# Kernel optimization log

Hardware: AMD Instinct MI355X
Metric: run time of the kernel (lower is better)

Reference implementation:

```python
import jax, jax.numpy as jnp
import numpy as np

N_NODES = 100000
N_EDGES = 1600000
NUM_GRAPHS = 64
IN_CH, HID, NUM_CLASSES = 128, 64, 10


def _glorot(key, fan_in, fan_out):
    scale = jnp.sqrt(2.0 / (fan_in + fan_out)).astype(jnp.float32)
    return jax.random.normal(key, (fan_in, fan_out), jnp.float32) * scale


def setup_inputs() -> dict:
    key = jax.random.key(0)
    ks = jax.random.split(key, 7)
    x = jax.random.normal(ks[0], (N_NODES, IN_CH), jnp.float32)
    edge_index = jax.random.randint(ks[1], (2, N_EDGES), 0, N_NODES, dtype=jnp.int32)
    batch = jnp.sort(jax.random.randint(ks[2], (N_NODES,), 0, NUM_GRAPHS, dtype=jnp.int32))
    return {
        "x": x,
        "edge_index": edge_index,
        "batch": batch,
        "W1": _glorot(ks[3], IN_CH, HID), "b1": jnp.zeros((HID,), jnp.float32),
        "W2": _glorot(ks[4], HID, HID), "b2": jnp.zeros((HID,), jnp.float32),
        "W3": _glorot(ks[5], HID, NUM_CLASSES), "b3": jnp.zeros((NUM_CLASSES,), jnp.float32),
    }


def _gcn_conv(x, src, dst, norm, W, b):
    # GCNConv: h = X W, then symmetric-normalized scatter-add over edges, then + b
    h = x @ W                                  # [N, out]
    msg = norm[:, None] * h[src]               # [E+N, out] gather
    out = jax.ops.segment_sum(msg, dst, num_segments=N_NODES)
    return out + b


def reference(x, edge_index, batch, W1, b1, W2, b2, W3, b3):
    loop = jnp.arange(N_NODES, dtype=edge_index.dtype)
    src = jnp.concatenate([edge_index[0], loop])   # self-loops added (PyG gcn_norm)
    dst = jnp.concatenate([edge_index[1], loop])
    deg = jax.ops.segment_sum(jnp.ones(src.shape[0], x.dtype), dst, num_segments=N_NODES)
    dinv = jnp.where(deg > 0, jax.lax.rsqrt(deg), jnp.zeros_like(deg))
    norm = dinv[src] * dinv[dst]

    h = jax.nn.relu(_gcn_conv(x, src, dst, norm, W1, b1))  # dropout is identity in eval
    h = jax.nn.relu(_gcn_conv(h, src, dst, norm, W2, b2))
    h = _gcn_conv(h, src, dst, norm, W3, b3)

    counts = jax.ops.segment_sum(jnp.ones(N_NODES, h.dtype), batch, num_segments=NUM_GRAPHS)
    pooled = jax.ops.segment_sum(h, batch, num_segments=NUM_GRAPHS) / jnp.maximum(counts, 1.0)[:, None]
    return jax.nn.log_softmax(pooled, axis=1)
```

## Files before the change

### kernel.cpp

```cpp
#include <hip/hip_runtime.h>
#include <math.h>

#define IN_CH 128
#define HID   64
#define NC    10
#define BSH   8
#define NBLK  256

typedef unsigned short bfu;
typedef __attribute__((ext_vector_type(8))) short bf16x8;
typedef __attribute__((ext_vector_type(4))) float f32x4;
typedef __attribute__((ext_vector_type(2))) float f32x2;

static __device__ __forceinline__ bfu bf16_of(float f) {
    unsigned u = __float_as_uint(f);
    unsigned r = (u + 0x7FFF + ((u >> 16) & 1)) >> 16;
    return (bfu)r;
}
static __device__ __forceinline__ float f_of_bf16(bfu u) {
    return __uint_as_float(((unsigned)u) << 16);
}

#if __has_builtin(__builtin_amdgcn_cvt_pk_f32_fp8) && __has_builtin(__builtin_amdgcn_cvt_pk_fp8_f32)
template <bool HI>
static __device__ __forceinline__ f32x2 fp8_unpk(unsigned d) {
    return __builtin_amdgcn_cvt_pk_f32_fp8((int)d, HI);
}
template <bool HI>
static __device__ __forceinline__ int fp8_pk(float a, float b, int old) {
    return __builtin_amdgcn_cvt_pk_fp8_f32(a, b, old, HI);
}
#else
static __device__ __forceinline__ float fp8_dec1(unsigned b) {
    unsigned s = b >> 7, e = (b >> 3) & 15, m = b & 7;
    float v = (e == 0) ? ldexpf((float)m, -9) : ldexpf((float)(8 + m), (int)e - 10);
    return s ? -v : v;
}
static __device__ __forceinline__ unsigned fp8_enc1(float f) {
    unsigned u = __float_as_uint(f);
    unsigned s = (u >> 31) << 7;
    f = fabsf(f);
    if (!(f < 448.f)) return s | 0x7E;
    if (f < 0.015625f) {
        int q = (int)rintf(f * 512.f);
        return s | (unsigned)q;
    }
    int e; float fr = frexpf(f, &e);
    int q = (int)rintf(fr * 16.f);
    if (q == 16) { q = 8; e++; }
    int E = e + 6;
    if (E >= 16) return s | 0x7E;
    return s | (unsigned)((E << 3) | (q - 8));
}
template <bool HI>
static __device__ __forceinline__ f32x2 fp8_unpk(unsigned d) {
    unsigned w = HI ? (d >> 16) : d;
    f32x2 r; r.x = fp8_dec1(w & 0xFF); r.y = fp8_dec1((w >> 8) & 0xFF);
    return r;
}
template <bool HI>
static __device__ __forceinline__ int fp8_pk(float a, float b, int old) {
    unsigned p = fp8_enc1(a) | (fp8_enc1(b) << 8);
    return HI ? (int)(((unsigned)old & 0x0000FFFFu) | (p << 16))
              : (int)(((unsigned)old & 0xFFFF0000u) | p);
}
#endif

__device__ __forceinline__ int lower_bound_i(const int* a, int n, int v) {
    int lo = 0, hi = n;
    while (lo < hi) { int mid = (lo + hi) >> 1; if (a[mid] < v) lo = mid + 1; else hi = mid; }
    return lo;
}


__global__ void k_init(int* __restrict__ cnt, float* __restrict__ Psum,
                       unsigned* __restrict__ dumA, unsigned* __restrict__ dumB,
                       int nbuck, int ng) {
    int t = threadIdx.x;
    for (int i = t; i < nbuck; i += 512) cnt[i] = 0;
    for (int i = t; i < ng * HID; i += 512) Psum[i] = 0.f;
    if (t < 16) { dumA[t] = 0u; dumB[t] = 0u; }
}


__global__ __launch_bounds__(1024) void k_part(const int* __restrict__ src,
                                               const int* __restrict__ dst,
                                               int* __restrict__ cnt,
                                               unsigned* __restrict__ packed,
                                               int E, int nbuck, int chunk, int cap) {
    __shared__ int hist[512];
    int tid = threadIdx.x;
    for (int b = tid; b < nbuck; b += 1024) hist[b] = 0;
    __syncthreads();
    int base = blockIdx.x * chunk;
    int lim  = min(base + chunk, E);
    for (int e = base + tid; e < lim; e += 1024)
        atomicAdd(&hist[dst[e] >> BSH], 1);
    __syncthreads();
    for (int b = tid; b < nbuck; b += 1024) {
        int c = hist[b];
        hist[b] = c ? atomicAdd(&cnt[b], c) : 0;
    }
    __syncthreads();
    for (int e = base + tid; e < lim; e += 1024) {
        int d = dst[e], s = src[e];
        int b = d >> BSH;
        int pos = atomicAdd(&hist[b], 1);
        if (pos < cap)
            packed[(size_t)b * (size_t)cap + pos] = ((unsigned)s << 8) | (unsigned)(d & 255);
    }
}


__global__ __launch_bounds__(512) void k_placeC(const unsigned* __restrict__ packed,
                                                const int* __restrict__ cnt,
                                                int2* __restrict__ rp2,
                                                float* __restrict__ dinv,
                                                int* __restrict__ meta,
                                                int nn, int cap, int capm) {
    __shared__ int hist[256];
    __shared__ int scn[256];
    __shared__ int cur[256];
    int tid = threadIdx.x;
    int b   = blockIdx.x;
    int nb0 = b << BSH;
    int nnb = min(1 << BSH, nn - nb0);
    if (tid < 256) hist[tid] = 0;
    __syncthreads();
    int lo = b * cap;
    int hi = lo + min(cnt[b], cap);
    for (int e = lo + tid; e < hi; e += blockDim.x)
        atomicAdd(&hist[packed[e] & 255u], 1);
    __syncthreads();
    int pd = 0;
    if (tid < 256) { pd = (hist[tid] + 3) & ~3; scn[tid] = pd; }
    __syncthreads();
    for (int off = 1; off < 256; off <<= 1) {
        int t = 0;
        if (tid < 256 && tid >= off) t = scn[tid - off];
        __syncthreads();
        if (tid < 256) scn[tid] += t;
        __syncthreads();
    }
    int meta0 = b * capm;
    if (tid < nnb) {
        int rp = meta0 + scn[tid] - pd;
        rp2[nb0 + tid] = make_int2(rp, rp + pd);
        cur[tid] = rp;
        dinv[nb0 + tid] = rsqrtf((float)(hist[tid] + 1));
        for (int k = hist[tid]; k < pd; k++) meta[rp + k] = nn;
    }
    __syncthreads();
    for (int e = lo + tid; e < hi; e += blockDim.x) {
        unsigned p = packed[e];
        int pos = atomicAdd(&cur[p & 255u], 1);
        meta[pos] = (int)(p >> 8);
    }
}


template <int K, bool IN_BF16>
__global__ __launch_bounds__(256) void k_gemm(const void* __restrict__ Xv,
                                              const float* __restrict__ W,
                                              const float* __restrict__ dinv,
                                              unsigned char* __restrict__ G8, int n) {
    constexpr int KS = K + 8;
    __shared__ bfu wt[64 * KS];
    int tid = threadIdx.x;
    for (int i = tid; i < K * 64; i += 256) {
        int k = i >> 6, nn2 = i & 63;
        wt[nn2 * KS + k] = bf16_of(W[i]);
    }
    __syncthreads();
    int wave = tid >> 6, lane = tid & 63;
    int m = lane & 15, q = lane >> 4;
    int row0 = blockIdx.x * 64 + wave * 16;
    int rowA = min(row0 + m, n - 1);
    f32x4 acc[4] = {{0.f,0.f,0.f,0.f},{0.f,0.f,0.f,0.f},
                    {0.f,0.f,0.f,0.f},{0.f,0.f,0.f,0.f}};
#pragma unroll
    for (int ks = 0; ks < K / 32; ks++) {
        bf16x8 a;
        if (IN_BF16) {
            a = *(const bf16x8*)((const bfu*)Xv + (size_t)rowA * 64 + ks * 32 + q * 8);
        } else {
            const float* xp = (const float*)Xv + (size_t)rowA * K + ks * 32 + q * 8;
            float4 v0 = *(const float4*)xp;
            float4 v1 = *(const float4*)(xp + 4);
            union { unsigned u[4]; bf16x8 v; } cvt;
            cvt.u[0] = __builtin_amdgcn_perm(__float_as_uint(v0.y), __float_as_uint(v0.x), 0x07060302u);
            cvt.u[1] = __builtin_amdgcn_perm(__float_as_uint(v0.w), __float_as_uint(v0.z), 0x07060302u);
            cvt.u[2] = __builtin_amdgcn_perm(__float_as_uint(v1.y), __float_as_uint(v1.x), 0x07060302u);
            cvt.u[3] = __builtin_amdgcn_perm(__float_as_uint(v1.w), __float_as_uint(v1.z), 0x07060302u);
            a = cvt.v;
        }
#pragma unroll
        for (int nt = 0; nt < 4; nt++) {
            bf16x8 b = *(const bf16x8*)&wt[(nt * 16 + m) * KS + ks * 32 + q * 8];
            acc[nt] = __builtin_amdgcn_mfma_f32_16x16x32_bf16(a, b, acc[nt], 0, 0, 0);
        }
    }
#pragma unroll
    for (int r = 0; r < 4; r++) {
        int grow = row0 + q * 4 + r;
        if (grow < n) {
            float dv = dinv[grow];
            int p01 = fp8_pk<false>(acc[0][r] * dv, acc[1][r] * dv, 0);
            int p23 = fp8_pk<false>(acc[2][r] * dv, acc[3][r] * dv, 0);
            unsigned char* gp = G8 + (size_t)grow * 64 + m;
            gp[0]  = (unsigned char)(p01 & 0xFF);
            gp[16] = (unsigned char)((p01 >> 8) & 0xFF);
            gp[32] = (unsigned char)(p23 & 0xFF);
            gp[48] = (unsigned char)((p23 >> 8) & 0xFF);
        }
    }
}


template <int MODE>
__global__ void k_agg(const unsigned* __restrict__ G4, const int* __restrict__ meta,
                      const int2* __restrict__ rp2, const float* __restrict__ dinv,
                      const float* __restrict__ bias, void* __restrict__ outv,
                      const int* __restrict__ batch, float* __restrict__ Psum,
                      int n, int ng, int do_relu, int post_scale) {
    __shared__ float pw[16][64];
    __shared__ int sb[16];
    int tid = threadIdx.x;
    int wbase = ((blockIdx.x * blockDim.x + tid) >> 6) * 4;
    if (MODE != 2) { if (wbase >= n) return; }
    int lane = tid & 63;
    int col4 = lane & 15, equad = lane >> 4;
    int nb0 = blockIdx.x * 16;
    if (MODE == 2 && tid < 16)
        sb[tid] = (nb0 + tid < n) ? batch[nb0 + tid] : -1;
    int nd    = wbase + equad;
    bool alive = nd < n;
    int ndc   = alive ? nd : (n - 1);
    int2 rp = rp2[ndc];
    int beg = rp.x, pend = alive ? rp.y : rp.x;
    f32x2 aA = {0.f, 0.f}, aB = {0.f, 0.f};
    for (int e = beg; e < pend; e += 4) {
        int4 m = *(const int4*)&meta[e];
        unsigned d0 = G4[(size_t)m.x * 16 + col4];
        unsigned d1 = G4[(size_t)m.y * 16 + col4];
        unsigned d2 = G4[(size_t)m.z * 16 + col4];
        unsigned d3 = G4[(size_t)m.w * 16 + col4];
        aA += fp8_unpk<false>(d0); aB += fp8_unpk<true>(d0);
        aA += fp8_unpk<false>(d1); aB += fp8_unpk<true>(d1);
        aA += fp8_unpk<false>(d2); aB += fp8_unpk<true>(d2);
        aA += fp8_unpk<false>(d3); aB += fp8_unpk<true>(d3);
    }
    unsigned sv = G4[(size_t)ndc * 16 + col4];
    aA += fp8_unpk<false>(sv); aB += fp8_unpk<true>(sv);
    float dv = dinv[ndc];
    float a0 = aA.x * dv, a1 = aA.y * dv, a2 = aB.x * dv, a3 = aB.y * dv;
    if (bias) {
        float4 bv = *(const float4*)&bias[col4 * 4];
        a0 += bv.x; a1 += bv.y; a2 += bv.z; a3 += bv.w;
    }
    if (do_relu) {
        a0 = fmaxf(a0, 0.f); a1 = fmaxf(a1, 0.f);
        a2 = fmaxf(a2, 0.f); a3 = fmaxf(a3, 0.f);
    }
    if (post_scale) { a0 *= dv; a1 *= dv; a2 *= dv; a3 *= dv; }
    if (MODE == 2) {
        int slot = (tid >> 6) * 4 + equad;
        f32x4 st;
        st.x = alive ? a0 : 0.f; st.y = alive ? a1 : 0.f;
        st.z = alive ? a2 : 0.f; st.w = alive ? a3 : 0.f;
        *(f32x4*)&pw[slot][col4 * 4] = st;
        __syncthreads();
        int r = tid >> 6, c = tid & 63;
        int g0 = sb[0];
        float v = 0.f;
#pragma unroll
        for (int s2 = 0; s2 < 16; s2++)
            if (sb[s2] == g0 + r) v += pw[s2][c];
        if (v != 0.f && g0 + r < ng) atomicAdd(&Psum[(g0 + r) * 64 + c], v);
        if (tid < 16) {
            int bb = sb[tid];
            if (bb > g0 + 3) {
                for (int c2 = 0; c2 < 64; c2++)
                    atomicAdd(&Psum[bb * 64 + c2], pw[tid][c2]);
            }
        }
    } else if (alive) {
        if (MODE == 1) {
            int p = fp8_pk<false>(a0, a1, 0);
            p = fp8_pk<true>(a2, a3, p);
            ((unsigned*)outv)[(size_t)nd * 16 + col4] = (unsigned)p;
        } else {
            uint2 o;
            o.x = (unsigned)bf16_of(a0) | ((unsigned)bf16_of(a1) << 16);
            o.y = (unsigned)bf16_of(a2) | ((unsigned)bf16_of(a3) << 16);
            ((uint2*)outv)[(size_t)nd * 16 + col4] = o;
        }
    }
}


__global__ void k_final(const float* __restrict__ Psum, const int* __restrict__ batch,
                        int n, const float* __restrict__ W3, const float* __restrict__ b3,
                        float* __restrict__ out, int ng) {
    __shared__ float P[64 * 64];
    __shared__ float s[64][NC];
    __shared__ float lse[64];
    __shared__ float invc[64];
    int t = threadIdx.x;
    if (t < ng) {
        int lo = lower_bound_i(batch, n, t);
        int hi = lower_bound_i(batch, n, t + 1);
        invc[t] = 1.f / (float)max(hi - lo, 1);
    }
    __syncthreads();
    for (int i = t; i < ng * 64; i += blockDim.x) P[i] = Psum[i] * invc[i >> 6];
    __syncthreads();
    if (t < ng * NC) {
        int g = t / NC, c = t % NC;
        float acc = b3[c];
        for (int k = 0; k < 64; k++) acc += P[g * 64 + k] * W3[k * NC + c];
        s[g][c] = acc;
    }
    __syncthreads();
    if (t < ng) {
        float m = -1e30f;
        for (int c = 0; c < NC; c++) m = fmaxf(m, s[t][c]);
        float sum = 0.f;
        for (int c = 0; c < NC; c++) sum += expf(s[t][c] - m);
        lse[t] = m + logf(sum);
    }
    __syncthreads();
    if (t < ng * NC) {
        int g = t / NC, c = t % NC;
        out[t] = s[g][c] - lse[g];
    }
}


extern "C" void kernel_launch(void* const* d_in, const int* in_sizes, int n_in,
                              void* d_out, int out_size, void* d_ws, size_t ws_size,
                              hipStream_t stream) {
    const float* x     = (const float*)d_in[0];
    const int*   ei    = (const int*)  d_in[1];
    const int*   batch = (const int*)  d_in[2];
    const float* W1    = (const float*)d_in[3];
    const float* b1    = (const float*)d_in[4];
    const float* W2    = (const float*)d_in[5];
    const float* b2    = (const float*)d_in[6];
    const float* W3    = (const float*)d_in[7];
    const float* b3    = (const float*)d_in[8];
    float*       out   = (float*)d_out;

    const int NN = in_sizes[0] / IN_CH;
    const int E  = in_sizes[1] / 2;
    const int NG = out_size / NC;
    const int nbuck = (NN + (1 << BSH) - 1) >> BSH;
    const int cap   = (int)(((((long long)E << BSH) / NN) + 768 + 3) & ~3LL);
    const int capm  = cap + 772;

    const int* src = ei;
    const int* dst = ei + E;

    char* ws = (char*)d_ws;
    size_t off = 0;
    auto carve = [&](size_t bytes) -> char* {
        char* p = ws + off;
        off = (off + bytes + 255) & ~(size_t)255;
        return p;
    };
    int2*  rp2    = (int2*) carve((size_t)NN * 8);
    float* dinv   = (float*)carve((size_t)NN * 4);
    int*   cnt    = (int*)  carve((size_t)nbuck * 4);
    int*   meta   = (int*)  carve(((size_t)nbuck * capm + 64) * 4);
    unsigned char* f8A = (unsigned char*)carve((size_t)(NN + 1) * 64);
    unsigned char* f8B = (unsigned char*)carve((size_t)(NN + 1) * 64);
    bfu*   hbuf   = (bfu*)  carve((size_t)NN * HID * 2);
    float* Psum   = (float*)carve((size_t)NG * HID * 4);
    (void)ws_size;

    unsigned* packed = (unsigned*)hbuf;

    const int chnk = (E + NBLK - 1) / NBLK;
    const int nbG  = (NN + 63) / 64;
    const int nbA  = (NN + 15) / 16;

    k_init<<<1, 512, 0, stream>>>(cnt, Psum,
                                  (unsigned*)(f8A + (size_t)NN * 64),
                                  (unsigned*)(f8B + (size_t)NN * 64), nbuck, NG);
    k_part<<<NBLK, 1024, 0, stream>>>(src, dst, cnt, packed, E, nbuck, chnk, cap);
    k_placeC<<<nbuck, 512, 0, stream>>>(packed, cnt, rp2, dinv, meta, NN, cap, capm);

    k_gemm<IN_CH, false><<<nbG, 256, 0, stream>>>(x, W1, dinv, f8A, NN);
    k_agg<0><<<nbA, 256, 0, stream>>>((const unsigned*)f8A, meta, rp2, dinv, b1,
                                      hbuf, nullptr, nullptr, NN, NG, 1, 0);
    k_gemm<HID, true><<<nbG, 256, 0, stream>>>(hbuf, W2, dinv, f8B, NN);
    k_agg<1><<<nbA, 256, 0, stream>>>((const unsigned*)f8B, meta, rp2, dinv, b2,
                                      f8A, nullptr, nullptr, NN, NG, 1, 1);
    k_agg<2><<<nbA, 256, 0, stream>>>((const unsigned*)f8A, meta, rp2, dinv, nullptr,
                                      nullptr, batch, Psum, NN, NG, 0, 0);
    k_final<<<1, 640, 0, stream>>>(Psum, batch, NN, W3, b3, out, NG);
}
```

Measured before the change: 249.5 us.

## Fuse layer-1 aggregation with layer-2 GEMM via in-block MFMA

```diff
diff --git a/kernel.cpp b/kernel.cpp
--- a/kernel.cpp
+++ b/kernel.cpp
@@ -16,9 +16,6 @@
     unsigned u = __float_as_uint(f);
     unsigned r = (u + 0x7FFF + ((u >> 16) & 1)) >> 16;
     return (bfu)r;
-}
-static __device__ __forceinline__ float f_of_bf16(bfu u) {
-    return __uint_as_float(((unsigned)u) << 16);
 }
 
 #if __has_builtin(__builtin_amdgcn_cvt_pk_f32_fp8) && __has_builtin(__builtin_amdgcn_cvt_pk_fp8_f32)
@@ -222,17 +219,26 @@
                       const int2* __restrict__ rp2, const float* __restrict__ dinv,
                       const float* __restrict__ bias, void* __restrict__ outv,
                       const int* __restrict__ batch, float* __restrict__ Psum,
+                      const float* __restrict__ Wg,
                       int n, int ng, int do_relu, int post_scale) {
-    __shared__ float pw[16][64];
-    __shared__ int sb[16];
+    extern __shared__ char smem[];
     int tid = threadIdx.x;
+    if (MODE == 3) {
+        bfu* wt = (bfu*)(smem + 16 * 72 * 2);
+        for (int i = tid; i < 64 * 64; i += 256) {
+            int k = i >> 6, c = i & 63;
+            wt[c * 72 + k] = bf16_of(Wg[i]);
+        }
+    }
     int wbase = ((blockIdx.x * blockDim.x + tid) >> 6) * 4;
-    if (MODE != 2) { if (wbase >= n) return; }
+    if (MODE == 1) { if (wbase >= n) return; }
     int lane = tid & 63;
     int col4 = lane & 15, equad = lane >> 4;
     int nb0 = blockIdx.x * 16;
-    if (MODE == 2 && tid < 16)
+    if (MODE == 2 && tid < 16) {
+        int* sb = (int*)(smem + 16 * 64 * 4);
         sb[tid] = (nb0 + tid < n) ? batch[nb0 + tid] : -1;
+    }
     int nd    = wbase + equad;
     bool alive = nd < n;
     int ndc   = alive ? nd : (n - 1);
@@ -263,38 +269,61 @@
         a2 = fmaxf(a2, 0.f); a3 = fmaxf(a3, 0.f);
     }
     if (post_scale) { a0 *= dv; a1 *= dv; a2 *= dv; a3 *= dv; }
-    if (MODE == 2) {
+    if (MODE == 3) {
+        bfu* pw = (bfu*)smem;
+        bfu* wt = (bfu*)(smem + 16 * 72 * 2);
+        int slot = (tid >> 6) * 4 + equad;
+        uint2 o;
+        o.x = (unsigned)bf16_of(alive ? a0 : 0.f) | ((unsigned)bf16_of(alive ? a1 : 0.f) << 16);
+        o.y = (unsigned)bf16_of(alive ? a2 : 0.f) | ((unsigned)bf16_of(alive ? a3 : 0.f) << 16);
+        *(uint2*)&pw[slot * 72 + col4 * 4] = o;
+        __syncthreads();
+        int w = tid >> 6, m = col4, q = equad;
+        f32x4 acc = {0.f, 0.f, 0.f, 0.f};
+#pragma unroll
+        for (int ks = 0; ks < 2; ks++) {
+            bf16x8 av = *(const bf16x8*)&pw[m * 72 + ks * 32 + q * 8];
+            bf16x8 bv = *(const bf16x8*)&wt[(w * 16 + m) * 72 + ks * 32 + q * 8];
+            acc = __builtin_amdgcn_mfma_f32_16x16x32_bf16(av, bv, acc, 0, 0, 0);
+        }
+        int c = w * 16 + m;
+        int r0 = nb0 + q * 4;
+        float dv0 = dinv[min(r0 + 0, n - 1)], dv1 = dinv[min(r0 + 1, n - 1)];
+        float dv2 = dinv[min(r0 + 2, n - 1)], dv3 = dinv[min(r0 + 3, n - 1)];
+        int p01 = fp8_pk<false>(acc[0] * dv0, acc[1] * dv1, 0);
+        int p23 = fp8_pk<false>(acc[2] * dv2, acc[3] * dv3, 0);
+        unsigned char* gp = (unsigned char*)outv;
+        if (r0 + 0 < n) gp[(size_t)(r0 + 0) * 64 + c] = (unsigned char)(p01 & 0xFF);
+        if (r0 + 1 < n) gp[(size_t)(r0 + 1) * 64 + c] = (unsigned char)((p01 >> 8) & 0xFF);
+        if (r0 + 2 < n) gp[(size_t)(r0 + 2) * 64 + c] = (unsigned char)(p23 & 0xFF);
+        if (r0 + 3 < n) gp[(size_t)(r0 + 3) * 64 + c] = (unsigned char)((p23 >> 8) & 0xFF);
+    } else if (MODE == 2) {
+        float* pwf = (float*)smem;
+        int*   sb  = (int*)(smem + 16 * 64 * 4);
         int slot = (tid >> 6) * 4 + equad;
         f32x4 st;
         st.x = alive ? a0 : 0.f; st.y = alive ? a1 : 0.f;
         st.z = alive ? a2 : 0.f; st.w = alive ? a3 : 0.f;
-        *(f32x4*)&pw[slot][col4 * 4] = st;
+        *(f32x4*)&pwf[slot * 64 + col4 * 4] = st;
         __syncthreads();
-        int r = tid >> 6, c = tid & 63;
+        int r = tid >> 6, cc = tid & 63;
         int g0 = sb[0];
         float v = 0.f;
 #pragma unroll
         for (int s2 = 0; s2 < 16; s2++)
-            if (sb[s2] == g0 + r) v += pw[s2][c];
-        if (v != 0.f && g0 + r < ng) atomicAdd(&Psum[(g0 + r) * 64 + c], v);
+            if (sb[s2] == g0 + r) v += pwf[s2 * 64 + cc];
+        if (v != 0.f && g0 + r < ng) atomicAdd(&Psum[(g0 + r) * 64 + cc], v);
         if (tid < 16) {
             int bb = sb[tid];
             if (bb > g0 + 3) {
                 for (int c2 = 0; c2 < 64; c2++)
-                    atomicAdd(&Psum[bb * 64 + c2], pw[tid][c2]);
+                    atomicAdd(&Psum[bb * 64 + c2], pwf[tid * 64 + c2]);
             }
         }
     } else if (alive) {
-        if (MODE == 1) {
-            int p = fp8_pk<false>(a0, a1, 0);
-            p = fp8_pk<true>(a2, a3, p);
-            ((unsigned*)outv)[(size_t)nd * 16 + col4] = (unsigned)p;
-        } else {
-            uint2 o;
-            o.x = (unsigned)bf16_of(a0) | ((unsigned)bf16_of(a1) << 16);
-            o.y = (unsigned)bf16_of(a2) | ((unsigned)bf16_of(a3) << 16);
-            ((uint2*)outv)[(size_t)nd * 16 + col4] = o;
-        }
+        int p = fp8_pk<false>(a0, a1, 0);
+        p = fp8_pk<true>(a2, a3, p);
+        ((unsigned*)outv)[(size_t)nd * 16 + col4] = (unsigned)p;
     }
 }
 
@@ -374,15 +403,16 @@
     int*   meta   = (int*)  carve(((size_t)nbuck * capm + 64) * 4);
     unsigned char* f8A = (unsigned char*)carve((size_t)(NN + 1) * 64);
     unsigned char* f8B = (unsigned char*)carve((size_t)(NN + 1) * 64);
-    bfu*   hbuf   = (bfu*)  carve((size_t)NN * HID * 2);
+    unsigned* packed = (unsigned*)carve((size_t)nbuck * cap * 4);
     float* Psum   = (float*)carve((size_t)NG * HID * 4);
     (void)ws_size;
-
-    unsigned* packed = (unsigned*)hbuf;
 
     const int chnk = (E + NBLK - 1) / NBLK;
     const int nbG  = (NN + 63) / 64;
     const int nbA  = (NN + 15) / 16;
+
+    const int smem3 = (16 * 72 + 64 * 72) * 2;
+    const int smem2 = 16 * 64 * 4 + 16 * 4;
 
     k_init<<<1, 512, 0, stream>>>(cnt, Psum,
                                   (unsigned*)(f8A + (size_t)NN * 64),
@@ -391,12 +421,11 @@
     k_placeC<<<nbuck, 512, 0, stream>>>(packed, cnt, rp2, dinv, meta, NN, cap, capm);
 
     k_gemm<IN_CH, false><<<nbG, 256, 0, stream>>>(x, W1, dinv, f8A, NN);
-    k_agg<0><<<nbA, 256, 0, stream>>>((const unsigned*)f8A, meta, rp2, dinv, b1,
-                                      hbuf, nullptr, nullptr, NN, NG, 1, 0);
-    k_gemm<HID, true><<<nbG, 256, 0, stream>>>(hbuf, W2, dinv, f8B, NN);
+    k_agg<3><<<nbA, 256, smem3, stream>>>((const unsigned*)f8A, meta, rp2, dinv, b1,
+                                          f8B, nullptr, nullptr, W2, NN, NG, 1, 0);
     k_agg<1><<<nbA, 256, 0, stream>>>((const unsigned*)f8B, meta, rp2, dinv, b2,
-                                      f8A, nullptr, nullptr, NN, NG, 1, 1);
-    k_agg<2><<<nbA, 256, 0, stream>>>((const unsigned*)f8A, meta, rp2, dinv, nullptr,
-                                      nullptr, batch, Psum, NN, NG, 0, 0);
+                                      f8A, nullptr, nullptr, nullptr, NN, NG, 1, 1);
+    k_agg<2><<<nbA, 256, smem2, stream>>>((const unsigned*)f8A, meta, rp2, dinv, nullptr,
+                                          nullptr, batch, Psum, nullptr, NN, NG, 0, 0);
     k_final<<<1, 640, 0, stream>>>(Psum, batch, NN, W3, b3, out, NG);
 }
```

Measured after the change: 246.4 us. About the same (-1.2%).
